# Kernel tuning notes

Hardware: AMD Instinct MI355X
Metric: run time of the kernel (lower is better)

The kernel has to match this reference:

```python
import jax, jax.numpy as jnp
import numpy as np

NEG = -1e30  # finite stand-in for -inf so logsumexp grads stay finite


def ctc_loss_mean(y_true, log_probs_tm, input_length, label_length, blank=0):
    """CTC loss (forward algorithm in log space), mean over batch.

    log_probs_tm: [T, B, C] time-major log-probabilities.
    y_true:       [B, L] dense int labels (blank=0 excluded from real labels).
    """
    T, B, C = log_probs_tm.shape
    L = y_true.shape[1]
    S = 2 * L + 1  # extended label length: blank, l1, blank, l2, ...
    ll = jnp.clip(label_length, 1, L)
    il = jnp.clip(input_length, 1, T)

    # Extended label sequence: blanks at even positions, labels at odd.
    ext = jnp.full((B, S), blank, dtype=jnp.int32).at[:, 1::2].set(y_true.astype(jnp.int32))
    ext_m2 = jnp.concatenate([jnp.full((B, 2), -1, jnp.int32), ext[:, :-2]], axis=1)
    # Skip transition (s-2 -> s) allowed only for label positions with no repeat.
    allow_skip = ((jnp.arange(S) % 2 == 1)[None, :]) & (ext != ext_m2)

    lp0 = jnp.take_along_axis(log_probs_tm[0], ext, axis=1)  # [B, S]
    alpha0 = jnp.full((B, S), NEG, log_probs_tm.dtype)
    alpha0 = alpha0.at[:, 0].set(lp0[:, 0]).at[:, 1].set(lp0[:, 1])

    def step(alpha, xs):
        lp_t, t = xs
        lpe = jnp.take_along_axis(lp_t, ext, axis=1)  # [B, S]
        a1 = jnp.concatenate([jnp.full((B, 1), NEG, alpha.dtype), alpha[:, :-1]], axis=1)
        a2 = jnp.concatenate([jnp.full((B, 2), NEG, alpha.dtype), alpha[:, :-2]], axis=1)
        a2 = jnp.where(allow_skip, a2, NEG)
        new = jax.nn.logsumexp(jnp.stack([alpha, a1, a2]), axis=0) + lpe
        # Freeze alpha once past each example's input_length.
        return jnp.where((t < il)[:, None], new, alpha), None

    alpha, _ = jax.lax.scan(step, alpha0, (log_probs_tm[1:], jnp.arange(1, T)))

    # Loss = -log(alpha[2*ll-1] + alpha[2*ll]) at the final (frozen) time step.
    idx = jnp.stack([2 * ll - 1, 2 * ll], axis=1)  # [B, 2]
    end_vals = jnp.take_along_axis(alpha, idx, axis=1)
    loss = -jax.nn.logsumexp(end_vals, axis=1)
    return jnp.mean(loss)


def setup_inputs() -> dict:
    key = jax.random.key(0)
    kx, kl, ki, kj = jax.random.split(key, 4)
    B, T, C, L = 64, 1024, 128, 256
    # y_pred are probabilities (module applies log), so softmax random logits.
    y_pred = jax.nn.softmax(jax.random.normal(kx, (B, T, C), jnp.float32), axis=-1)
    y_true = jax.random.randint(kl, (B, L), 1, C, jnp.int32)  # blank=0 excluded
    input_length = jax.random.randint(ki, (B,), T // 2, T + 1, jnp.int32)
    label_length = jax.random.randint(kj, (B,), L // 2, L + 1, jnp.int32)
    return {"y_true": y_true, "y_pred": y_pred,
            "input_length": input_length, "label_length": label_length}


def reference(y_true, y_pred, input_length, label_length):
    # Mirror CTCLayer.call: log + transpose to time-major, reshape lengths.
    log_tm = jnp.log(jnp.transpose(y_pred, (1, 0, 2)))  # [T, B, C]
    loss = ctc_loss_mean(y_true, log_tm,
                         input_length.reshape(-1), label_length.reshape(-1),
                         blank=0)
    return log_tm, loss
```

## Files before the change

### kernel.cpp

```cpp
#include <hip/hip_runtime.h>
#include <math.h>

constexpr int B = 64;
constexpr int T = 1024;
constexpr int C = 128;
constexpr int L = 256;
constexpr int S = 2 * L + 1;
constexpr int TRB = 2048;

template <int N> struct IC { static constexpr int value = N; };

__device__ __forceinline__ float shr1(float x) {
    return __int_as_float(__builtin_amdgcn_update_dpp(
        0, __float_as_int(x), 0x138 , 0xf, 0xf, false));
}

template <int CTRL>
__device__ __forceinline__ float maxdpp(float x) {
    float t = __int_as_float(__builtin_amdgcn_update_dpp(
        __float_as_int(x), __float_as_int(x), CTRL, 0xf, 0xf, false));
    return fmaxf(x, t);
}

__device__ __forceinline__ float wave_max_dpp(float x) {
    x = maxdpp<0x111>(x);
    x = maxdpp<0x112>(x);
    x = maxdpp<0x114>(x);
    x = maxdpp<0x118>(x);
    x = maxdpp<0x142>(x);
    x = maxdpp<0x143>(x);
    return __int_as_float(__builtin_amdgcn_readlane(__float_as_int(x), 63));
}

__global__ __launch_bounds__(64, 1) void ctc_fused(
    const float* __restrict__ yp,
    const int*   __restrict__ yt,
    const int*   __restrict__ il_,
    const int*   __restrict__ ll_,
    float* __restrict__ out_log,
    float* __restrict__ out_loss)
{
    const int lane = threadIdx.x;
    if (blockIdx.x >= B) {
        int id = blockIdx.x - B;
        int bb = id >> 5;
        int ck = id & 31;
        const float4* src = (const float4*)yp + ((size_t)bb * T + ck * 32) * 32;
        float4* o4 = (float4*)out_log;
        #pragma unroll
        for (int k = 0; k < 16; ++k) {
            int o = k * 64 + lane;
            float4 v = src[o];
            int tt = ck * 32 + (o >> 5);
            int c4 = o & 31;
            float4 r;
            r.x = __logf(v.x); r.y = __logf(v.y);
            r.z = __logf(v.z); r.w = __logf(v.w);
            o4[((size_t)tt * B + bb) * 32 + c4] = r;
        }
        return;
    }

    const int b = blockIdx.x;

    __shared__ float lsh[2048];
    __shared__ float afin[S];

    int il = il_[b]; il = min(max(il, 1), T);
    int ll = ll_[b]; ll = min(max(ll, 1), L);
    const float* yb = yp + (size_t)b * T * C;

    int4 y4  = *(const int4*)(yt + b * L + 4 * lane);
    int  po  = lane ? 4 * lane - 4 : 0;
    int4 py4 = *(const int4*)(yt + b * L + po);
    int  ppw = yt[b * L + (lane >= 2 ? 4 * lane - 5 : 0)];

    int lab[8]   = {py4.x, py4.y, py4.z, py4.w, y4.x, y4.y, y4.z, y4.w};
    int labm1[8] = {ppw,   py4.x, py4.y, py4.z, py4.w, y4.x, y4.y, y4.z};
    float skf[8];
    #pragma unroll
    for (int k = 0; k < 8; ++k)
        skf[k] = ((4 * lane + k >= 5) && (lab[k] != labm1[k])) ? 1.f : 0.f;

    const int c0 = y4.x, c1 = y4.y, c2 = y4.z, c3 = y4.w;

    auto ldpair = [&](int m) -> float4 {
        int r = 2 * m + 1 + (lane >> 5);
        r = r > T - 1 ? T - 1 : r;
        return ((const float4*)(yb + (size_t)r * C))[lane & 31];
    };

    float p00 = yb[0];
    float p0l = yb[c0];

    float4 q0 = ldpair(0), q1 = ldpair(1);
    float4 q2 = ldpair(2), q3 = ldpair(3);
    float4 prr[8];
    #pragma unroll
    for (int m = 4; m <= 11; ++m) prr[m & 7] = ldpair(m);

    ((float4*)(lsh +   0))[lane] = q0;
    ((float4*)(lsh + 256))[lane] = q1;
    ((float4*)(lsh + 512))[lane] = q2;
    ((float4*)(lsh + 768))[lane] = q3;

    float gv[4][4][4], gbv[4][4];
    #pragma unroll
    for (int q = 0; q < 2; ++q)
        #pragma unroll
        for (int j = 0; j < 4; ++j) {
            const float* base = lsh + q * 512 + j * 128;
            gbv[q][j] = base[0];
            gv[q][j][0] = base[c0]; gv[q][j][1] = base[c1];
            gv[q][j][2] = base[c2]; gv[q][j][3] = base[c3];
        }

    float w[17];
    #pragma unroll
    for (int i = 0; i < 17; ++i) w[i] = 0.f;
    if (lane == 0) { w[8] = p00; w[9] = p0l; }

    auto halo = [&]() {
        #pragma unroll
        for (int k = 0; k < 8; ++k) w[k] = shr1(w[8 + k]);
    };
    halo();

    int lsi = 0;
    int t0 = 0;

    auto group = [&](auto Pc, auto S0c) {
        constexpr int P  = decltype(Pc)::value;
        constexpr int S0 = decltype(S0c)::value;
        constexpr int BF = (P + 2) & 3;
        float g1[4], g2[4], g3[4];
        #pragma unroll
        for (int j = 0; j < 4; ++j) {
            g1[j] = shr1(gv[P][j][1]);
            g2[j] = shr1(gv[P][j][2]);
            g3[j] = shr1(gv[P][j][3]);
        }
        #pragma unroll
        for (int j = 0; j < 4; ++j) {
            #pragma unroll
            for (int i = 16; i >= 2 * (j + 1); --i) {
                float acc = w[i] + w[i - 1];
                float g;
                if (i & 1) {
                    const int k = (i - 1) >> 1;
                    acc = fmaf(skf[k], w[i - 2], acc);
                    g = (k >= 4) ? gv[P][j][k - 4]
                                 : (k == 1 ? g1[j] : (k == 2 ? g2[j] : g3[j]));
                } else {
                    g = gbv[P][j];
                }
                w[i] = acc * g;
            }
        }
        ((float4*)(lsh + BF * 512      ))[lane] = prr[S0];
        ((float4*)(lsh + BF * 512 + 256))[lane] = prr[S0 + 1];
        prr[S0]     = ldpair((t0 >> 1) + 12);
        prr[S0 + 1] = ldpair((t0 >> 1) + 13);
        #pragma unroll
        for (int j = 0; j < 4; ++j) {
            const float* base = lsh + BF * 512 + j * 128;
            gbv[BF][j] = base[0];
            gv[BF][j][0] = base[c0]; gv[BF][j][1] = base[c1];
            gv[BF][j][2] = base[c2]; gv[BF][j][3] = base[c3];
        }
        halo();
        t0 += 4;
    };

    auto maxw = [&]() {
        return fmaxf(fmaxf(fmaxf(w[8], w[9]), fmaxf(w[10], w[11])),
                     fmaxf(fmaxf(w[12], w[13]),
                           fmaxf(fmaxf(w[14], w[15]), w[16])));
    };
    auto rescale = [&]() {
        float mm = wave_max_dpp(maxw());
        int eb = (__float_as_int(mm) >> 23) & 0xff;
        int sh = 350 - eb;
        sh = sh > 254 ? 254 : (sh < 1 ? 1 : sh);
        float inv = __int_as_float(sh << 23);
        #pragma unroll
        for (int i = 8; i < 17; ++i) w[i] *= inv;
        lsi -= sh - 127;
    };

    const int full_end = ((il - 1) >> 2) << 2;

    while (t0 + 16 <= full_end) {
        group(IC<0>{}, IC<4>{});
        group(IC<1>{}, IC<6>{});
        rescale();
        group(IC<2>{}, IC<0>{});
        group(IC<3>{}, IC<2>{});
        rescale();
    }

    if (t0 + 4 <= full_end) { group(IC<0>{}, IC<4>{}); rescale(); }
    if (t0 + 4 <= full_end) { group(IC<1>{}, IC<6>{}); rescale(); }
    if (t0 + 4 <= full_end) { group(IC<2>{}, IC<0>{}); }

    const int ph = (full_end >> 2) & 3;
    float tg[3][4], tb[3];
    switch (ph) {
    case 0:
        #pragma unroll
        for (int j = 0; j < 3; ++j) { tb[j]=gbv[0][j]; tg[j][0]=gv[0][j][0]; tg[j][1]=gv[0][j][1]; tg[j][2]=gv[0][j][2]; tg[j][3]=gv[0][j][3]; }
        break;
    case 1:
        #pragma unroll
        for (int j = 0; j < 3; ++j) { tb[j]=gbv[1][j]; tg[j][0]=gv[1][j][0]; tg[j][1]=gv[1][j][1]; tg[j][2]=gv[1][j][2]; tg[j][3]=gv[1][j][3]; }
        break;
    case 2:
        #pragma unroll
        for (int j = 0; j < 3; ++j) { tb[j]=gbv[2][j]; tg[j][0]=gv[2][j][0]; tg[j][1]=gv[2][j][1]; tg[j][2]=gv[2][j][2]; tg[j][3]=gv[2][j][3]; }
        break;
    default:
        #pragma unroll
        for (int j = 0; j < 3; ++j) { tb[j]=gbv[3][j]; tg[j][0]=gv[3][j][0]; tg[j][1]=gv[3][j][1]; tg[j][2]=gv[3][j][2]; tg[j][3]=gv[3][j][3]; }
        break;
    }
    #pragma unroll
    for (int j = 0; j < 3; ++j) {
        int r = full_end + 1 + j;
        if (r < il) {
            float hh = shr1(w[15]);
            float gb = tb[j];
            float n8  = (w[8] + hh) * gb;
            float n9  = fmaf(skf[4], hh,    w[9]  + w[8])  * tg[j][0];
            float n10 = (w[10] + w[9])  * gb;
            float n11 = fmaf(skf[5], w[9],  w[11] + w[10]) * tg[j][1];
            float n12 = (w[12] + w[11]) * gb;
            float n13 = fmaf(skf[6], w[11], w[13] + w[12]) * tg[j][2];
            float n14 = (w[14] + w[13]) * gb;
            float n15 = fmaf(skf[7], w[13], w[15] + w[14]) * tg[j][3];
            float n16 = (w[16] + w[15]) * gb;
            w[8] = n8;  w[9] = n9;  w[10] = n10; w[11] = n11; w[12] = n12;
            w[13] = n13; w[14] = n14; w[15] = n15; w[16] = n16;
        }
    }

    #pragma unroll
    for (int k = 0; k < 8; ++k) afin[8 * lane + k] = w[8 + k];
    if (lane == 63) afin[512] = w[16];
    __syncthreads();
    if (lane == 0) {
        float e1 = afin[2 * ll - 1];
        float e2 = afin[2 * ll];
        float sum = fmaxf(e1 + e2, 1e-37f);
        float loss = -(__log2f(sum) + (float)lsi) * 0.6931471805599453f;
        atomicAdd(out_loss, loss * (1.0f / (float)B));
    }
}

extern "C" void kernel_launch(void* const* d_in, const int* in_sizes, int n_in,
                              void* d_out, int out_size, void* d_ws, size_t ws_size,
                              hipStream_t stream) {
    const int*   y_true = (const int*)d_in[0];
    const float* y_pred = (const float*)d_in[1];
    const int*   in_len = (const int*)d_in[2];
    const int*   lb_len = (const int*)d_in[3];

    float* out_log  = (float*)d_out;
    float* out_loss = (float*)d_out + (size_t)T * B * C;

    hipMemsetAsync(out_loss, 0, sizeof(float), stream);
    ctc_fused<<<B + TRB, 64, 0, stream>>>(y_pred, y_true, in_len, lb_len,
                                          out_log, out_loss);
}
```

Measured before the change: 187.0 us.

## Split CTC into prep kernel pre-gathering label probs and forward recurrence kernel

Adds a separate prep kernel that writes the log output and also gathers, for every batch and time step, the probabilities at each lane's four labels into a workspace array, plus a blank-probability column. The forward kernel then streams contiguous per-lane float4 gathers from the workspace instead of staging full rows in LDS and doing indexed LDS reads each step. This removes LDS gather latency from the serial recurrence. In exchange it adds a second kernel launch, a serialization point between the kernels, and extra global traffic of B*T*256 floats written and read back.

After: 203.5 us. 1.09x slower.

```diff
diff --git a/kernel.cpp b/kernel.cpp
--- a/kernel.cpp
+++ b/kernel.cpp
@@ -6,7 +6,6 @@
 constexpr int C = 128;
 constexpr int L = 256;
 constexpr int S = 2 * L + 1;
-constexpr int TRB = 2048;
 
 template <int N> struct IC { static constexpr int value = N; };
 
@@ -32,49 +31,63 @@
     return __int_as_float(__builtin_amdgcn_readlane(__float_as_int(x), 63));
 }
 
-__global__ __launch_bounds__(64, 1) void ctc_fused(
+__global__ __launch_bounds__(256) void ctc_prep(
     const float* __restrict__ yp,
+    const int*   __restrict__ yt,
+    float* __restrict__ out_log,
+    float* __restrict__ glab,
+    float* __restrict__ bc)
+{
+    const int bb   = blockIdx.x >> 4;
+    const int ck   = blockIdx.x & 15;
+    const int wv   = threadIdx.x >> 6;
+    const int lane = threadIdx.x & 63;
+
+    __shared__ float rowbuf[4][2][128];
+
+    int4 ly = *(const int4*)(yt + bb * L + 4 * lane);
+    const int tbase = ck * 64 + wv * 16;
+
+    for (int i = 0; i < 16; ++i) {
+        const int t = tbase + i;
+        const float2 v = ((const float2*)(yp + ((size_t)bb * T + t) * C))[lane];
+        ((float2*)rowbuf[wv][i & 1])[lane] = v;
+        float2 lg; lg.x = __logf(v.x); lg.y = __logf(v.y);
+        ((float2*)(out_log + ((size_t)t * B + bb) * C))[lane] = lg;
+        if (lane == 0) bc[bb * T + t] = v.x;
+        const float* rb = rowbuf[wv][i & 1];
+        float4 g;
+        g.x = rb[ly.x]; g.y = rb[ly.y]; g.z = rb[ly.z]; g.w = rb[ly.w];
+        ((float4*)(glab + ((size_t)bb * T + t) * 256))[lane] = g;
+    }
+}
+
+__global__ __launch_bounds__(64, 1) void ctc_fwd(
+    const float* __restrict__ glab,
+    const float* __restrict__ bc,
     const int*   __restrict__ yt,
     const int*   __restrict__ il_,
     const int*   __restrict__ ll_,
-    float* __restrict__ out_log,
     float* __restrict__ out_loss)
 {
+    const int b    = blockIdx.x;
     const int lane = threadIdx.x;
-    if (blockIdx.x >= B) {
-        int id = blockIdx.x - B;
-        int bb = id >> 5;
-        int ck = id & 31;
-        const float4* src = (const float4*)yp + ((size_t)bb * T + ck * 32) * 32;
-        float4* o4 = (float4*)out_log;
-        #pragma unroll
-        for (int k = 0; k < 16; ++k) {
-            int o = k * 64 + lane;
-            float4 v = src[o];
-            int tt = ck * 32 + (o >> 5);
-            int c4 = o & 31;
-            float4 r;
-            r.x = __logf(v.x); r.y = __logf(v.y);
-            r.z = __logf(v.z); r.w = __logf(v.w);
-            o4[((size_t)tt * B + bb) * 32 + c4] = r;
-        }
-        return;
-    }
-
-    const int b = blockIdx.x;
-
-    __shared__ float lsh[2048];
+
+    __shared__ float blanks[T];
     __shared__ float afin[S];
 
     int il = il_[b]; il = min(max(il, 1), T);
     int ll = ll_[b]; ll = min(max(ll, 1), L);
-    const float* yb = yp + (size_t)b * T * C;
+    const float* gb_base = glab + (size_t)b * T * 256;
+
+    #pragma unroll
+    for (int i = 0; i < T / 64; ++i)
+        blanks[i * 64 + lane] = bc[b * T + i * 64 + lane];
 
     int4 y4  = *(const int4*)(yt + b * L + 4 * lane);
     int  po  = lane ? 4 * lane - 4 : 0;
     int4 py4 = *(const int4*)(yt + b * L + po);
     int  ppw = yt[b * L + (lane >= 2 ? 4 * lane - 5 : 0)];
-
     int lab[8]   = {py4.x, py4.y, py4.z, py4.w, y4.x, y4.y, y4.z, y4.w};
     int labm1[8] = {ppw,   py4.x, py4.y, py4.z, py4.w, y4.x, y4.y, y4.z};
     float skf[8];
@@ -82,63 +95,41 @@
     for (int k = 0; k < 8; ++k)
         skf[k] = ((4 * lane + k >= 5) && (lab[k] != labm1[k])) ? 1.f : 0.f;
 
-    const int c0 = y4.x, c1 = y4.y, c2 = y4.z, c3 = y4.w;
-
-    auto ldpair = [&](int m) -> float4 {
-        int r = 2 * m + 1 + (lane >> 5);
-        r = r > T - 1 ? T - 1 : r;
-        return ((const float4*)(yb + (size_t)r * C))[lane & 31];
-    };
-
-    float p00 = yb[0];
-    float p0l = yb[c0];
-
-    float4 q0 = ldpair(0), q1 = ldpair(1);
-    float4 q2 = ldpair(2), q3 = ldpair(3);
-    float4 prr[8];
-    #pragma unroll
-    for (int m = 4; m <= 11; ++m) prr[m & 7] = ldpair(m);
-
-    ((float4*)(lsh +   0))[lane] = q0;
-    ((float4*)(lsh + 256))[lane] = q1;
-    ((float4*)(lsh + 512))[lane] = q2;
-    ((float4*)(lsh + 768))[lane] = q3;
-
-    float gv[4][4][4], gbv[4][4];
-    #pragma unroll
-    for (int q = 0; q < 2; ++q)
-        #pragma unroll
-        for (int j = 0; j < 4; ++j) {
-            const float* base = lsh + q * 512 + j * 128;
-            gbv[q][j] = base[0];
-            gv[q][j][0] = base[c0]; gv[q][j][1] = base[c1];
-            gv[q][j][2] = base[c2]; gv[q][j][3] = base[c3];
-        }
+    float4 rr[16];
+    #pragma unroll
+    for (int r = 1; r <= 16; ++r)
+        rr[r & 15] = ((const float4*)(gb_base + (size_t)r * 256))[lane];
+
+    float g00 = gb_base[0];
 
     float w[17];
     #pragma unroll
     for (int i = 0; i < 17; ++i) w[i] = 0.f;
-    if (lane == 0) { w[8] = p00; w[9] = p0l; }
+    if (lane == 0) { w[8] = blanks[0]; w[9] = g00; }
 
     auto halo = [&]() {
         #pragma unroll
         for (int k = 0; k < 8; ++k) w[k] = shr1(w[8 + k]);
     };
     halo();
+
+    float gbc[4];
+    #pragma unroll
+    for (int j = 0; j < 4; ++j) gbc[j] = blanks[1 + j];
 
     int lsi = 0;
     int t0 = 0;
 
-    auto group = [&](auto Pc, auto S0c) {
-        constexpr int P  = decltype(Pc)::value;
-        constexpr int S0 = decltype(S0c)::value;
-        constexpr int BF = (P + 2) & 3;
+    auto group = [&](auto Pc) {
+        constexpr int P = decltype(Pc)::value;
+        float4 gj[4] = { rr[(4 * P + 1) & 15], rr[(4 * P + 2) & 15],
+                         rr[(4 * P + 3) & 15], rr[(4 * P + 4) & 15] };
         float g1[4], g2[4], g3[4];
         #pragma unroll
         for (int j = 0; j < 4; ++j) {
-            g1[j] = shr1(gv[P][j][1]);
-            g2[j] = shr1(gv[P][j][2]);
-            g3[j] = shr1(gv[P][j][3]);
+            g1[j] = shr1(gj[j].y);
+            g2[j] = shr1(gj[j].z);
+            g3[j] = shr1(gj[j].w);
         }
         #pragma unroll
         for (int j = 0; j < 4; ++j) {
@@ -149,24 +140,25 @@
                 if (i & 1) {
                     const int k = (i - 1) >> 1;
                     acc = fmaf(skf[k], w[i - 2], acc);
-                    g = (k >= 4) ? gv[P][j][k - 4]
-                                 : (k == 1 ? g1[j] : (k == 2 ? g2[j] : g3[j]));
+                    g = (k == 4) ? gj[j].x : (k == 5) ? gj[j].y :
+                        (k == 6) ? gj[j].z : (k == 7) ? gj[j].w :
+                        (k == 1) ? g1[j]   : (k == 2) ? g2[j] : g3[j];
                 } else {
-                    g = gbv[P][j];
+                    g = gbc[j];
                 }
                 w[i] = acc * g;
             }
         }
-        ((float4*)(lsh + BF * 512      ))[lane] = prr[S0];
-        ((float4*)(lsh + BF * 512 + 256))[lane] = prr[S0 + 1];
-        prr[S0]     = ldpair((t0 >> 1) + 12);
-        prr[S0 + 1] = ldpair((t0 >> 1) + 13);
-        #pragma unroll
-        for (int j = 0; j < 4; ++j) {
-            const float* base = lsh + BF * 512 + j * 128;
-            gbv[BF][j] = base[0];
-            gv[BF][j][0] = base[c0]; gv[BF][j][1] = base[c1];
-            gv[BF][j][2] = base[c2]; gv[BF][j][3] = base[c3];
+        #pragma unroll
+        for (int j = 0; j < 4; ++j) {
+            int r = t0 + 17 + j; r = r > T - 1 ? T - 1 : r;
+            rr[(4 * P + 1 + j) & 15] =
+                ((const float4*)(gb_base + (size_t)r * 256))[lane];
+        }
+        #pragma unroll
+        for (int j = 0; j < 4; ++j) {
+            int r = t0 + 5 + j; r = r > T - 1 ? T - 1 : r;
+            gbc[j] = blanks[r];
         }
         halo();
         t0 += 4;
@@ -191,52 +183,39 @@
     const int full_end = ((il - 1) >> 2) << 2;
 
     while (t0 + 16 <= full_end) {
-        group(IC<0>{}, IC<4>{});
-        group(IC<1>{}, IC<6>{});
+        group(IC<0>{});
+        group(IC<1>{});
         rescale();
-        group(IC<2>{}, IC<0>{});
-        group(IC<3>{}, IC<2>{});
+        group(IC<2>{});
+        group(IC<3>{});
         rescale();
     }
-
-    if (t0 + 4 <= full_end) { group(IC<0>{}, IC<4>{}); rescale(); }
-    if (t0 + 4 <= full_end) { group(IC<1>{}, IC<6>{}); rescale(); }
-    if (t0 + 4 <= full_end) { group(IC<2>{}, IC<0>{}); }
+    if (t0 + 4 <= full_end) { group(IC<0>{}); rescale(); }
+    if (t0 + 4 <= full_end) { group(IC<1>{}); rescale(); }
+    if (t0 + 4 <= full_end) { group(IC<2>{}); }
 
     const int ph = (full_end >> 2) & 3;
-    float tg[3][4], tb[3];
+    float4 tg[3];
     switch (ph) {
-    case 0:
-        #pragma unroll
-        for (int j = 0; j < 3; ++j) { tb[j]=gbv[0][j]; tg[j][0]=gv[0][j][0]; tg[j][1]=gv[0][j][1]; tg[j][2]=gv[0][j][2]; tg[j][3]=gv[0][j][3]; }
-        break;
-    case 1:
-        #pragma unroll
-        for (int j = 0; j < 3; ++j) { tb[j]=gbv[1][j]; tg[j][0]=gv[1][j][0]; tg[j][1]=gv[1][j][1]; tg[j][2]=gv[1][j][2]; tg[j][3]=gv[1][j][3]; }
-        break;
-    case 2:
-        #pragma unroll
-        for (int j = 0; j < 3; ++j) { tb[j]=gbv[2][j]; tg[j][0]=gv[2][j][0]; tg[j][1]=gv[2][j][1]; tg[j][2]=gv[2][j][2]; tg[j][3]=gv[2][j][3]; }
-        break;
-    default:
-        #pragma unroll
-        for (int j = 0; j < 3; ++j) { tb[j]=gbv[3][j]; tg[j][0]=gv[3][j][0]; tg[j][1]=gv[3][j][1]; tg[j][2]=gv[3][j][2]; tg[j][3]=gv[3][j][3]; }
-        break;
+    case 0:  tg[0]=rr[1];  tg[1]=rr[2];  tg[2]=rr[3];  break;
+    case 1:  tg[0]=rr[5];  tg[1]=rr[6];  tg[2]=rr[7];  break;
+    case 2:  tg[0]=rr[9];  tg[1]=rr[10]; tg[2]=rr[11]; break;
+    default: tg[0]=rr[13]; tg[1]=rr[14]; tg[2]=rr[15]; break;
     }
     #pragma unroll
     for (int j = 0; j < 3; ++j) {
         int r = full_end + 1 + j;
         if (r < il) {
             float hh = shr1(w[15]);
-            float gb = tb[j];
+            float gb = blanks[r];
             float n8  = (w[8] + hh) * gb;
-            float n9  = fmaf(skf[4], hh,    w[9]  + w[8])  * tg[j][0];
+            float n9  = fmaf(skf[4], hh,    w[9]  + w[8])  * tg[j].x;
             float n10 = (w[10] + w[9])  * gb;
-            float n11 = fmaf(skf[5], w[9],  w[11] + w[10]) * tg[j][1];
+            float n11 = fmaf(skf[5], w[9],  w[11] + w[10]) * tg[j].y;
             float n12 = (w[12] + w[11]) * gb;
-            float n13 = fmaf(skf[6], w[11], w[13] + w[12]) * tg[j][2];
+            float n13 = fmaf(skf[6], w[11], w[13] + w[12]) * tg[j].z;
             float n14 = (w[14] + w[13]) * gb;
-            float n15 = fmaf(skf[7], w[13], w[15] + w[14]) * tg[j][3];
+            float n15 = fmaf(skf[7], w[13], w[15] + w[14]) * tg[j].w;
             float n16 = (w[16] + w[15]) * gb;
             w[8] = n8;  w[9] = n9;  w[10] = n10; w[11] = n11; w[12] = n12;
             w[13] = n13; w[14] = n14; w[15] = n15; w[16] = n16;
@@ -267,7 +246,10 @@
     float* out_log  = (float*)d_out;
     float* out_loss = (float*)d_out + (size_t)T * B * C;
 
+    float* glab = (float*)d_ws;
+    float* bcol = glab + (size_t)B * T * 256;
+
     hipMemsetAsync(out_loss, 0, sizeof(float), stream);
-    ctc_fused<<<B + TRB, 64, 0, stream>>>(y_pred, y_true, in_len, lb_len,
-                                          out_log, out_loss);
-}
+    ctc_prep<<<B * 16, 256, 0, stream>>>(y_pred, y_true, out_log, glab, bcol);
+    ctc_fwd<<<B, 64, 0, stream>>>(glab, bcol, y_true, in_len, lb_len, out_loss);
+}
```
